# Kernel tuning notes

Hardware: AMD Instinct MI355X
Metric: run time of the kernel (lower is better)

The kernel has to match this reference:

```python
import jax, jax.numpy as jnp
import numpy as np

REP_THR = 0.6
BORDER = 10


def setup_inputs() -> dict:
    key = jax.random.key(0)
    repeatability = jax.random.uniform(key, (8, 1, 2048, 2048), dtype=jnp.float32)
    return {"repeatability": repeatability}


def reference(repeatability):
    # 3x3 max pool, stride 1, pad 1 (torch pads with -inf for max pool)
    local_max = jax.lax.reduce_window(
        repeatability,
        -jnp.inf,
        jax.lax.max,
        window_dimensions=(1, 1, 3, 3),
        window_strides=(1, 1, 1, 1),
        padding=[(0, 0), (0, 0), (1, 1), (1, 1)],
    )
    maxima = (repeatability == local_max) & (repeatability >= REP_THR)
    # border mask: zero out a 10-pixel frame
    B, C, H, W = repeatability.shape
    border = jnp.zeros((H, W), dtype=bool).at[BORDER:-BORDER, BORDER:-BORDER].set(True)
    maxima = maxima & border  # broadcast over (B, C)
    # Original returns maxima.nonzero().t()[2:4] (data-dependent shape);
    # for jit-compatibility we return the dense boolean mask as float32 —
    # the (y, x) indices are exactly the nonzero positions of this mask.
    return maxima.astype(jnp.float32)
```

## Files before the change

### kernel.cpp

```cpp
#include <hip/hip_runtime.h>
#include <math.h>

#define IMG_H 2048
#define IMG_W 2048
#define NB    8
#define BORDER 10
#define REP_THR 0.6f

__global__ __launch_bounds__(256) void nms_kernel(const float* __restrict__ in,
                                                  float* __restrict__ out) {
    const int tid = blockIdx.x * blockDim.x + threadIdx.x;
    const int gx = tid & 511;
    const int gy = (tid >> 9) & 511;
    const int b  = tid >> 18;

    const int x4 = gx << 2;
    const int y0 = gy << 2;

    const size_t img_off = (size_t)b * IMG_H * IMG_W;
    float* obase = out + img_off + (size_t)y0 * IMG_W + x4;

    if (y0 + 4 <= BORDER || y0 >= IMG_H - BORDER || gx == 0 || gx == 511) {
        const float4 z = make_float4(0.f, 0.f, 0.f, 0.f);
        *(float4*)(obase + 0 * IMG_W) = z;
        *(float4*)(obase + 1 * IMG_W) = z;
        *(float4*)(obase + 2 * IMG_W) = z;
        *(float4*)(obase + 3 * IMG_W) = z;
        return;
    }

    const float* base = in + img_off + (size_t)(y0 - 1) * IMG_W + x4;

    float4 h[6];
    float4 c[4];
#pragma unroll
    for (int r = 0; r < 6; ++r) {
        const float* row = base + (size_t)r * IMG_W;
        const float4 v = *(const float4*)row;
        const float  l = row[-1];
        const float  q = row[4];
        float4 hh;
        hh.x = fmaxf(l,   fmaxf(v.x, v.y));
        hh.y = fmaxf(v.x, fmaxf(v.y, v.z));
        hh.z = fmaxf(v.y, fmaxf(v.z, v.w));
        hh.w = fmaxf(v.z, fmaxf(v.w, q));
        h[r] = hh;
        if (r >= 1 && r <= 4) c[r - 1] = v;
    }

    const bool bx0 = (x4 + 0 >= BORDER) && (x4 + 0 < IMG_W - BORDER);
    const bool bx1 = (x4 + 1 >= BORDER) && (x4 + 1 < IMG_W - BORDER);
    const bool bx2 = (x4 + 2 >= BORDER) && (x4 + 2 < IMG_W - BORDER);
    const bool bx3 = (x4 + 3 >= BORDER) && (x4 + 3 < IMG_W - BORDER);

#pragma unroll
    for (int j = 0; j < 4; ++j) {
        const int y = y0 + j;
        const bool rowok = (y >= BORDER) && (y < IMG_H - BORDER);

        float4 m;
        m.x = fmaxf(h[j].x, fmaxf(h[j + 1].x, h[j + 2].x));
        m.y = fmaxf(h[j].y, fmaxf(h[j + 1].y, h[j + 2].y));
        m.z = fmaxf(h[j].z, fmaxf(h[j + 1].z, h[j + 2].z));
        m.w = fmaxf(h[j].w, fmaxf(h[j + 1].w, h[j + 2].w));

        float4 r;
        r.x = (c[j].x == m.x && c[j].x >= REP_THR && bx0 && rowok) ? 1.f : 0.f;
        r.y = (c[j].y == m.y && c[j].y >= REP_THR && bx1 && rowok) ? 1.f : 0.f;
        r.z = (c[j].z == m.z && c[j].z >= REP_THR && bx2 && rowok) ? 1.f : 0.f;
        r.w = (c[j].w == m.w && c[j].w >= REP_THR && bx3 && rowok) ? 1.f : 0.f;

        *(float4*)(obase + (size_t)j * IMG_W) = r;
    }
}

extern "C" void kernel_launch(void* const* d_in, const int* in_sizes, int n_in,
                              void* d_out, int out_size, void* d_ws, size_t ws_size,
                              hipStream_t stream) {
    const float* in = (const float*)d_in[0];
    float* out = (float*)d_out;
    const int total_threads = NB * (IMG_H / 4) * (IMG_W / 4);
    const int block = 256;
    const int grid = total_threads / block;
    nms_kernel<<<grid, block, 0, stream>>>(in, out);
}
```

Baseline: 226.1 us.

## Process 16-row strips per thread with rolling row window and nontemporal stores

Each thread now handles a 4x16 strip instead of 4x4 and slides a three-row window of horizontal maxima down the strip. This cuts the vertical halo re-reads from 6 rows per 4 outputs to 18 per 16. Row indices are clamped to the border range, so border-row threads no longer take a separate zero path, and output is written with nontemporal stores. The trade-off is a 4x smaller grid with more serial work per thread, which lowers the parallelism available to hide memory latency.

```diff
diff --git a/kernel.cpp b/kernel.cpp
--- a/kernel.cpp
+++ b/kernel.cpp
@@ -6,47 +6,52 @@
 #define NB    8
 #define BORDER 10
 #define REP_THR 0.6f
+#define ROWS 16
+
+typedef float f32x4 __attribute__((ext_vector_type(4)));
 
 __global__ __launch_bounds__(256) void nms_kernel(const float* __restrict__ in,
                                                   float* __restrict__ out) {
     const int tid = blockIdx.x * blockDim.x + threadIdx.x;
-    const int gx = tid & 511;
-    const int gy = (tid >> 9) & 511;
-    const int b  = tid >> 18;
+    const int gx  = tid & 511;
+    const int gys = (tid >> 9) & 127;
+    const int b   = tid >> 16;
 
     const int x4 = gx << 2;
-    const int y0 = gy << 2;
+    const int y0 = gys << 4;
 
     const size_t img_off = (size_t)b * IMG_H * IMG_W;
     float* obase = out + img_off + (size_t)y0 * IMG_W + x4;
 
-    if (y0 + 4 <= BORDER || y0 >= IMG_H - BORDER || gx == 0 || gx == 511) {
-        const float4 z = make_float4(0.f, 0.f, 0.f, 0.f);
-        *(float4*)(obase + 0 * IMG_W) = z;
-        *(float4*)(obase + 1 * IMG_W) = z;
-        *(float4*)(obase + 2 * IMG_W) = z;
-        *(float4*)(obase + 3 * IMG_W) = z;
+    if (gx == 0 || gx == 511) {
+        const f32x4 z = {0.f, 0.f, 0.f, 0.f};
+#pragma unroll
+        for (int j = 0; j < ROWS; ++j)
+            __builtin_nontemporal_store(z, (f32x4*)(obase + (size_t)j * IMG_W));
         return;
     }
 
-    const float* base = in + img_off + (size_t)(y0 - 1) * IMG_W + x4;
+    const float* ibase = in + img_off + x4;
+    const int rlo = BORDER - 1;
+    const int rhi = IMG_H - BORDER;
 
-    float4 h[6];
-    float4 c[4];
-#pragma unroll
-    for (int r = 0; r < 6; ++r) {
-        const float* row = base + (size_t)r * IMG_W;
-        const float4 v = *(const float4*)row;
-        const float  l = row[-1];
-        const float  q = row[4];
-        float4 hh;
-        hh.x = fmaxf(l,   fmaxf(v.x, v.y));
-        hh.y = fmaxf(v.x, fmaxf(v.y, v.z));
-        hh.z = fmaxf(v.y, fmaxf(v.z, v.w));
-        hh.w = fmaxf(v.z, fmaxf(v.w, q));
-        h[r] = hh;
-        if (r >= 1 && r <= 4) c[r - 1] = v;
-    }
+#define LOADROW(r, v, h) do {                                             \
+        int rc_ = (r);                                                    \
+        rc_ = rc_ < rlo ? rlo : (rc_ > rhi ? rhi : rc_);                  \
+        const float* row_ = ibase + (size_t)rc_ * IMG_W;                  \
+        (v) = *(const f32x4*)row_;                                        \
+        const float l_ = row_[-1];                                        \
+        const float q_ = row_[4];                                         \
+        (h)[0] = fmaxf(l_,     fmaxf((v)[0], (v)[1]));                    \
+        (h)[1] = fmaxf((v)[0], fmaxf((v)[1], (v)[2]));                    \
+        (h)[2] = fmaxf((v)[1], fmaxf((v)[2], (v)[3]));                    \
+        (h)[3] = fmaxf((v)[2], fmaxf((v)[3], q_));                        \
+    } while (0)
+
+    f32x4 vA, hA, vB, hB;
+    LOADROW(y0 - 1, vA, hA);
+    LOADROW(y0,     vB, hB);
+    (void)vA;
 
     const bool bx0 = (x4 + 0 >= BORDER) && (x4 + 0 < IMG_W - BORDER);
     const bool bx1 = (x4 + 1 >= BORDER) && (x4 + 1 < IMG_W - BORDER);
@@ -54,24 +59,33 @@
     const bool bx3 = (x4 + 3 >= BORDER) && (x4 + 3 < IMG_W - BORDER);
 
 #pragma unroll
-    for (int j = 0; j < 4; ++j) {
+    for (int j = 0; j < ROWS; ++j) {
         const int y = y0 + j;
+
+        f32x4 vC, hC;
+        LOADROW(y + 1, vC, hC);
+
+        f32x4 m;
+        m[0] = fmaxf(hA[0], fmaxf(hB[0], hC[0]));
+        m[1] = fmaxf(hA[1], fmaxf(hB[1], hC[1]));
+        m[2] = fmaxf(hA[2], fmaxf(hB[2], hC[2]));
+        m[3] = fmaxf(hA[3], fmaxf(hB[3], hC[3]));
+
         const bool rowok = (y >= BORDER) && (y < IMG_H - BORDER);
 
-        float4 m;
-        m.x = fmaxf(h[j].x, fmaxf(h[j + 1].x, h[j + 2].x));
-        m.y = fmaxf(h[j].y, fmaxf(h[j + 1].y, h[j + 2].y));
-        m.z = fmaxf(h[j].z, fmaxf(h[j + 1].z, h[j + 2].z));
-        m.w = fmaxf(h[j].w, fmaxf(h[j + 1].w, h[j + 2].w));
+        f32x4 r;
+        r[0] = (vB[0] == m[0] && vB[0] >= REP_THR && bx0 && rowok) ? 1.f : 0.f;
+        r[1] = (vB[1] == m[1] && vB[1] >= REP_THR && bx1 && rowok) ? 1.f : 0.f;
+        r[2] = (vB[2] == m[2] && vB[2] >= REP_THR && bx2 && rowok) ? 1.f : 0.f;
+        r[3] = (vB[3] == m[3] && vB[3] >= REP_THR && bx3 && rowok) ? 1.f : 0.f;
 
-        float4 r;
-        r.x = (c[j].x == m.x && c[j].x >= REP_THR && bx0 && rowok) ? 1.f : 0.f;
-        r.y = (c[j].y == m.y && c[j].y >= REP_THR && bx1 && rowok) ? 1.f : 0.f;
-        r.z = (c[j].z == m.z && c[j].z >= REP_THR && bx2 && rowok) ? 1.f : 0.f;
-        r.w = (c[j].w == m.w && c[j].w >= REP_THR && bx3 && rowok) ? 1.f : 0.f;
+        __builtin_nontemporal_store(r, (f32x4*)(obase + (size_t)j * IMG_W));
 
-        *(float4*)(obase + (size_t)j * IMG_W) = r;
+        hA = hB;
+        vB = vC;
+        hB = hC;
     }
+#undef LOADROW
 }
 
 extern "C" void kernel_launch(void* const* d_in, const int* in_sizes, int n_in,
@@ -79,7 +93,7 @@
                               hipStream_t stream) {
     const float* in = (const float*)d_in[0];
     float* out = (float*)d_out;
-    const int total_threads = NB * (IMG_H / 4) * (IMG_W / 4);
+    const int total_threads = NB * (IMG_H / ROWS) * (IMG_W / 4);
     const int block = 256;
     const int grid = total_threads / block;
     nms_kernel<<<grid, block, 0, stream>>>(in, out);
```

Measured after the change: 235.7 us. 1.04x slower.
